# Optimization experiments

Measured on AMD Instinct MI355X. Metric: run time of the kernel, lower is better.

Reference implementation:

```python
import jax, jax.numpy as jnp
import numpy as np

# Forest of B perfect binary trees, depth D levels, M = 2**D - 1 nodes/tree.
B, D, H, X, VOCAB, NCLS = 32, 12, 256, 256, 32000, 20
M = 2 ** D - 1          # 4095 nodes per tree
N = B * M               # 131040 total nodes


def setup_inputs() -> dict:
    key = jax.random.key(0)
    ks = jax.random.split(key, 9)
    x = jax.random.randint(ks[0], (N,), 0, VOCAB, dtype=jnp.int32)
    # leaves are the last level of each tree: in-tree index >= 2**(D-1)-1
    leaf = (jnp.arange(M) >= 2 ** (D - 1) - 1).astype(jnp.int32)
    x_mask = jnp.tile(leaf, B)  # [N] int32, 1 on leaves, 0 on internal nodes
    s = 0.02
    Emb = jax.random.normal(ks[1], (VOCAB, X), jnp.float32) * s
    W_iou = jax.random.normal(ks[2], (3 * H, X), jnp.float32) * s
    b_iou = jnp.zeros((3 * H,), jnp.float32)
    U_iou = jax.random.normal(ks[3], (3 * H, H), jnp.float32) * s
    U_f = jax.random.normal(ks[4], (H, H), jnp.float32) * s
    b_f = jnp.ones((H,), jnp.float32)  # forget-gate bias init
    W_out = jax.random.normal(ks[5], (NCLS, H), jnp.float32) * s
    b_out = jnp.zeros((NCLS,), jnp.float32)
    return {"x": x, "x_mask": x_mask, "Emb": Emb, "W_iou": W_iou,
            "b_iou": b_iou, "U_iou": U_iou, "U_f": U_f, "b_f": b_f,
            "W_out": W_out, "b_out": b_out}


def reference(x, x_mask, Emb, W_iou, b_iou, U_iou, U_f, b_f, W_out, b_out):
    # input_module: embedding applied to masked ids, result masked again
    x_emb = Emb[x * x_mask] * x_mask[:, None].astype(Emb.dtype)      # [N, X]
    xiou = (x_emb @ W_iou.T).reshape(B, M, 3 * H)                    # W_iou * x per node
    h_sum = jnp.zeros((B, M, H), Emb.dtype)    # sum of children h (childsum)
    fc_sum = jnp.zeros((B, M, H), Emb.dtype)   # sum_k f_k * c_k from children
    h_all = jnp.zeros((B, M, H), Emb.dtype)
    # topological propagation: leaves (deepest level) -> roots
    for l in range(D - 1, -1, -1):
        s_, e_ = 2 ** l - 1, 2 ** (l + 1) - 1  # static in-tree level slice
        iou = xiou[:, s_:e_] + h_sum[:, s_:e_] @ U_iou.T + b_iou
        i, o, u = jnp.split(iou, 3, axis=-1)
        c = jax.nn.sigmoid(i) * jnp.tanh(u) + fc_sum[:, s_:e_]
        h = jax.nn.sigmoid(o) * jnp.tanh(c)
        h_all = h_all.at[:, s_:e_].set(h)
        if l > 0:
            f = jax.nn.sigmoid(h @ U_f.T + b_f)          # per-child forget gate
            parents = (np.arange(s_, e_) - 1) // 2       # static parent indices
            h_sum = h_sum.at[:, parents].add(h)
            fc_sum = fc_sum.at[:, parents].add(f * c)
    # output_module applied to all node states
    return h_all.reshape(N, H) @ W_out.T + b_out                    # [N, NCLS]
```

## Files before the change

### kernel.cpp

```cpp
#include <hip/hip_runtime.h>

#define B_TREES 32
#define DEPTH   12
#define M_NODES 4095
#define N_NODES (B_TREES * M_NODES)
#define HDIM    256
#define VOCAB   32000
#define NCLS    20
#define LEAFROWS 65536
#define LDSH_S 20

typedef _Float16 f16;
typedef _Float16 f16x8 __attribute__((ext_vector_type(8)));
typedef _Float16 f16x4 __attribute__((ext_vector_type(4)));
typedef _Float16 f16x2 __attribute__((ext_vector_type(2)));
typedef float    f32x4 __attribute__((ext_vector_type(4)));

__device__ __forceinline__ float sigf(float x)      { return 1.0f / (1.0f + __expf(-x)); }
__device__ __forceinline__ float tanh_fast(float x) { return 1.0f - 2.0f / (1.0f + __expf(2.0f * x)); }

__global__ __launch_bounds__(256) void cvt_kernel(
    const float4* __restrict__ Emb,  const float4* __restrict__ Wiou,
    const float4* __restrict__ Uiou, const float4* __restrict__ Uf,
    const float4* __restrict__ Wout,
    f16x4* __restrict__ Emb16,  f16x4* __restrict__ Wiou16,
    f16x4* __restrict__ Uiou16, f16x4* __restrict__ Uf16,
    f16x4* __restrict__ Wout16)
{
    int i = blockIdx.x * 256 + threadIdx.x;
    if (i < VOCAB * HDIM / 4) {
        float4 v = Emb[i];
        f16x4 r; r[0] = (f16)v.x; r[1] = (f16)v.y; r[2] = (f16)v.z; r[3] = (f16)v.w;
        Emb16[i] = r;
    }
    if (i < 768 * HDIM / 4) {
        float4 v = Wiou[i];
        f16x4 r; r[0] = (f16)v.x; r[1] = (f16)v.y; r[2] = (f16)v.z; r[3] = (f16)v.w;
        Wiou16[i] = r;
        float4 u = Uiou[i];
        f16x4 s; s[0] = (f16)u.x; s[1] = (f16)u.y; s[2] = (f16)u.z; s[3] = (f16)u.w;
        Uiou16[i] = s;
    }
    if (i < HDIM * HDIM / 4) {
        float4 v = Uf[i];
        f16x4 r; r[0] = (f16)v.x; r[1] = (f16)v.y; r[2] = (f16)v.z; r[3] = (f16)v.w;
        Uf16[i] = r;
    }
    if (i < 32 * HDIM / 4) {
        int row = i >> 6;
        f16x4 r = {};
        if (row < NCLS) {
            float4 v = Wout[i];
            r[0] = (f16)v.x; r[1] = (f16)v.y; r[2] = (f16)v.z; r[3] = (f16)v.w;
        }
        Wout16[i] = r;
    }
}

#define LEAF_TPW 8
__global__ __launch_bounds__(256) void leaf_kernel(
    const int* __restrict__ x, const f16* __restrict__ Emb16,
    const f16* __restrict__ Wiou16, const float* __restrict__ b_iou,
    f16* __restrict__ h16, f16* __restrict__ cT)
{
    __shared__ f16 wlds[1536 * 8];
    __shared__ f16 ldsh[4][16 * LDSH_S];

    const int tid  = threadIdx.x;
    const int lane = tid & 63;
    const int w    = tid >> 6;
    const int quad = lane >> 4;
    const int l15  = lane & 15;
    const int qk   = quad * 8;
    const int cb0  = blockIdx.y * 16;

    #pragma unroll
    for (int i = 0; i < 6; ++i) {
        int f = i * 256 + tid;
        int mat = f >> 9, r = f & 511, ks = r >> 6, q = (r >> 4) & 3, c = r & 15;
        *(f16x8*)(wlds + f * 8) = *(const f16x8*)(Wiou16 +
            (mat * 256 + cb0 + c) * HDIM + ks * 32 + q * 8);
    }
    __syncthreads();

    const float bi = b_iou[cb0 + l15];
    const float bo = b_iou[256 + cb0 + l15];
    const float bu = b_iou[512 + cb0 + l15];

    const int row0 = (blockIdx.x * 4 + w) * (LEAF_TPW * 16);

    int nodeRow = (row0 >> 11) * M_NODES + 2047 + (row0 & 2047);
    int embBase = x[nodeRow + l15] * HDIM;
    f16x8 a[8];
    #pragma unroll
    for (int ks = 0; ks < 8; ++ks)
        a[ks] = *(const f16x8*)(Emb16 + embBase + ks * 32 + qk);

    for (int rt = 0; rt < LEAF_TPW; ++rt) {
        const int rw = row0 + rt * 16;
        const int curNode = nodeRow;
        f16x8 ac[8];
        #pragma unroll
        for (int ks = 0; ks < 8; ++ks) ac[ks] = a[ks];

        if (rt + 1 < LEAF_TPW) {
            const int rwn = rw + 16;
            nodeRow = (rwn >> 11) * M_NODES + 2047 + (rwn & 2047);
            embBase = x[nodeRow + l15] * HDIM;
            #pragma unroll
            for (int ks = 0; ks < 8; ++ks)
                a[ks] = *(const f16x8*)(Emb16 + embBase + ks * 32 + qk);
        }

        f32x4 acc[3] = {};
        #pragma unroll
        for (int ks = 0; ks < 8; ++ks) {
            #pragma unroll
            for (int mat = 0; mat < 3; ++mat) {
                f16x8 wf = *(const f16x8*)(wlds +
                    ((mat * 8 + ks) * 64 + quad * 16 + l15) * 8);
                acc[mat] = __builtin_amdgcn_mfma_f32_16x16x32_f16(
                    ac[ks], wf, acc[mat], 0, 0, 0);
            }
        }

        f16x4 cv;
        #pragma unroll
        for (int r = 0; r < 4; ++r) {
            float i_ = acc[0][r] + bi;
            float o_ = acc[1][r] + bo;
            float u_ = acc[2][r] + bu;
            float c  = sigf(i_) * tanh_fast(u_);
            float h  = sigf(o_) * tanh_fast(c);
            cv[r] = (f16)c;
            ldsh[w][(quad * 4 + r) * LDSH_S + l15] = (f16)h;
        }
        *(f16x4*)(cT + (cb0 + l15) * LEAFROWS + rw + quad * 4) = cv;

        {
            int row_l = lane >> 2, cpos = (lane & 3) * 4;
            f16x4 v = *(const f16x4*)(&ldsh[w][row_l * LDSH_S + cpos]);
            *(f16x4*)(h16 + (curNode + row_l) * HDIM + cb0 + cpos) = v;
        }
    }
}

__global__ __launch_bounds__(256) void fused_level_kernel(
    const f16* __restrict__ Uiou16, const f16* __restrict__ Uf16,
    const float* __restrict__ b_iou, const float* __restrict__ b_f,
    f16* __restrict__ h16, const f16* __restrict__ cT_child,
    f16* __restrict__ cT_parent, int l, int rows_p, int tpw)
{
    __shared__ f16 wlds[2048 * 8];
    __shared__ f16 ldsh[4][16 * LDSH_S];

    const int tid  = threadIdx.x;
    const int lane = tid & 63;
    const int w    = tid >> 6;
    const int quad = lane >> 4;
    const int l15  = lane & 15;
    const int qk   = quad * 8;
    const int cb0  = blockIdx.y * 16;

    #pragma unroll
    for (int i = 0; i < 8; ++i) {
        int f = i * 256 + tid;
        int mat = f >> 9, r = f & 511, ks = r >> 6, q = (r >> 4) & 3, c = r & 15;
        const f16* src = (mat == 0)
            ? (Uf16 + (cb0 + c) * HDIM + ks * 32 + q * 8)
            : (Uiou16 + ((mat - 1) * 256 + cb0 + c) * HDIM + ks * 32 + q * 8);
        *(f16x8*)(wlds + f * 8) = *(const f16x8*)src;
    }
    __syncthreads();

    const float bi  = b_iou[cb0 + l15];
    const float bo  = b_iou[256 + cb0 + l15];
    const float bu  = b_iou[512 + cb0 + l15];
    const float bfv = b_f[cb0 + l15];
    const int lc = l + 1;
    const int maskc = (1 << lc) - 1;
    const int maskp = (1 << l) - 1;
    const int rows_c = rows_p * 2;

    const int p0 = blockIdx.x * (tpw * 64);

    for (int pt = 0; pt < tpw; ++pt) {
        const int pw = p0 + (pt * 4 + w) * 16;
        if (pw >= rows_p) continue;
        const int cw = 2 * pw;

        int childBase0, childBase1;
        {
            int cl0 = cw + l15;
            childBase0 = ((cl0 >> lc) * M_NODES + maskc + (cl0 & maskc)) * HDIM;
            int cl1 = cw + 16 + l15;
            childBase1 = ((cl1 >> lc) * M_NODES + maskc + (cl1 & maskc)) * HDIM;
        }

        f32x4 accf0 = {}, accf1 = {};
        f32x4 au0[3] = {}, au1[3] = {};
        #pragma unroll
        for (int ks = 0; ks < 8; ++ks) {
            const int k0 = ks * 32 + qk;
            f16x8 a0 = *(const f16x8*)(h16 + childBase0 + k0);
            f16x8 a1 = *(const f16x8*)(h16 + childBase1 + k0);
            f16x8 wfF = *(const f16x8*)(wlds + (ks * 64 + quad * 16 + l15) * 8);
            accf0 = __builtin_amdgcn_mfma_f32_16x16x32_f16(a0, wfF, accf0, 0, 0, 0);
            accf1 = __builtin_amdgcn_mfma_f32_16x16x32_f16(a1, wfF, accf1, 0, 0, 0);
            #pragma unroll
            for (int m = 0; m < 3; ++m) {
                f16x8 wm = *(const f16x8*)(wlds +
                    (((m + 1) * 8 + ks) * 64 + quad * 16 + l15) * 8);
                au0[m] = __builtin_amdgcn_mfma_f32_16x16x32_f16(a0, wm, au0[m], 0, 0, 0);
                au1[m] = __builtin_amdgcn_mfma_f32_16x16x32_f16(a1, wm, au1[m], 0, 0, 0);
            }
        }

        #pragma unroll
        for (int s = 0; s < 2; ++s) {
            const f32x4& af = s ? accf1 : accf0;
            const f32x4* au = s ? au1 : au0;
            const int csr = cw + s * 16;
            f16x4 cc = *(const f16x4*)(cT_child +
                (cb0 + l15) * rows_c + csr + quad * 4);
            f16x2 cpack;
            #pragma unroll
            for (int pr = 0; pr < 2; ++pr) {
                float f0 = sigf(af[2 * pr]     + bfv);
                float f1 = sigf(af[2 * pr + 1] + bfv);
                float fc = f0 * (float)cc[2 * pr] + f1 * (float)cc[2 * pr + 1];
                float i_ = au[0][2 * pr] + au[0][2 * pr + 1] + bi;
                float o_ = au[1][2 * pr] + au[1][2 * pr + 1] + bo;
                float u_ = au[2][2 * pr] + au[2][2 * pr + 1] + bu;
                float c  = sigf(i_) * tanh_fast(u_) + fc;
                float h  = sigf(o_) * tanh_fast(c);
                cpack[pr] = (f16)c;
                ldsh[w][(s * 8 + quad * 2 + pr) * LDSH_S + l15] = (f16)h;
            }
            *(f16x2*)(cT_parent + (cb0 + l15) * rows_p + pw + s * 8 + quad * 2) = cpack;
        }

        {
            int prow = lane >> 2, cpos = (lane & 3) * 4;
            int p = pw + prow;
            int b = p >> l, tt = p & maskp;
            int node = b * M_NODES + (1 << l) - 1 + tt;
            f16x4 v = *(const f16x4*)(&ldsh[w][prow * LDSH_S + cpos]);
            *(f16x4*)(h16 + node * HDIM + cb0 + cpos) = v;
        }
    }
}

__global__ __launch_bounds__(256) void out_kernel(
    const f16* __restrict__ h16, const f16* __restrict__ Wout16,
    const float* __restrict__ bout, float* __restrict__ out)
{
    const int lane = threadIdx.x & 63;
    const int w    = threadIdx.x >> 6;
    const int quad = lane >> 4;
    const int l15  = lane & 15;
    const int qk   = quad * 8;

    f16x8 wfk[2][8];
    #pragma unroll
    for (int cf = 0; cf < 2; ++cf)
        #pragma unroll
        for (int ks = 0; ks < 8; ++ks)
            wfk[cf][ks] = *(const f16x8*)(Wout16 +
                (cf * 16 + l15) * HDIM + ks * 32 + qk);
    float bo[2];
    #pragma unroll
    for (int cf = 0; cf < 2; ++cf) {
        int col = cf * 16 + l15;
        bo[cf] = bout[col < NCLS ? col : 0];
    }

    const int tile0  = blockIdx.x * 16;
    const int ntotal = N_NODES / 16;
    const int tend   = (tile0 + 16 < ntotal) ? 16 : (ntotal - tile0);

    for (int rt = w; rt < tend; rt += 4) {
        const int rw = (tile0 + rt) * 16;
        f32x4 acc[2] = {};
        #pragma unroll
        for (int ks = 0; ks < 8; ++ks) {
            f16x8 a = *(const f16x8*)(h16 + (rw + l15) * HDIM + ks * 32 + qk);
            #pragma unroll
            for (int cf = 0; cf < 2; ++cf)
                acc[cf] = __builtin_amdgcn_mfma_f32_16x16x32_f16(
                    a, wfk[cf][ks], acc[cf], 0, 0, 0);
        }
        #pragma unroll
        for (int cf = 0; cf < 2; ++cf) {
            const int col = cf * 16 + l15;
            if (col < NCLS) {
                #pragma unroll
                for (int r = 0; r < 4; ++r)
                    out[(rw + quad * 4 + r) * NCLS + col] = acc[cf][r] + bo[cf];
            }
        }
    }
}

extern "C" void kernel_launch(void* const* d_in, const int* in_sizes, int n_in,
                              void* d_out, int out_size, void* d_ws, size_t ws_size,
                              hipStream_t stream)
{
    const int*   x     = (const int*)d_in[0];
    const float* Emb   = (const float*)d_in[2];
    const float* W_iou = (const float*)d_in[3];
    const float* b_iou = (const float*)d_in[4];
    const float* U_iou = (const float*)d_in[5];
    const float* U_f   = (const float*)d_in[6];
    const float* b_f   = (const float*)d_in[7];
    const float* W_out = (const float*)d_in[8];
    const float* b_out = (const float*)d_in[9];
    float* out = (float*)d_out;

    char* ws = (char*)d_ws;
    size_t off = 0;
    auto take = [&](size_t bytes) -> char* {
        char* p = ws + off; off += (bytes + 255) & ~(size_t)255; return p;
    };
    f16* h16    = (f16*)take((size_t)N_NODES * HDIM * 2);
    f16* cA     = (f16*)take((size_t)HDIM * LEAFROWS * 2);
    f16* cB     = (f16*)take((size_t)HDIM * (LEAFROWS / 2) * 2);
    f16* Emb16  = (f16*)take((size_t)VOCAB * HDIM * 2);
    f16* Wiou16 = (f16*)take((size_t)768 * HDIM * 2);
    f16* Uiou16 = (f16*)take((size_t)768 * HDIM * 2);
    f16* Uf16   = (f16*)take((size_t)HDIM * HDIM * 2);
    f16* Wout16 = (f16*)take((size_t)32 * HDIM * 2);

    cvt_kernel<<<VOCAB * HDIM / 4 / 256, 256, 0, stream>>>(
        (const float4*)Emb, (const float4*)W_iou, (const float4*)U_iou,
        (const float4*)U_f, (const float4*)W_out,
        (f16x4*)Emb16, (f16x4*)Wiou16, (f16x4*)Uiou16, (f16x4*)Uf16,
        (f16x4*)Wout16);

    leaf_kernel<<<dim3(LEAFROWS / (4 * 16 * LEAF_TPW), 16), 256, 0, stream>>>(
        x, Emb16, Wiou16, b_iou, h16, cA);

    f16* cin  = cA;
    f16* cout_ = cB;
    for (int l = 10; l >= 0; --l) {
        int rows_p = B_TREES << l;
        int tpw = rows_p / (64 * 128); if (tpw < 1) tpw = 1;
        int gx  = (rows_p + tpw * 64 - 1) / (tpw * 64);
        fused_level_kernel<<<dim3(gx, 16), 256, 0, stream>>>(
            Uiou16, Uf16, b_iou, b_f, h16, cin, cout_, l, rows_p, tpw);
        f16* t = cin; cin = cout_; cout_ = t;
    }

    out_kernel<<<dim3((N_NODES / 16 + 15) / 16), 256, 0, stream>>>(
        h16, Wout16, b_out, out);
}
```

Baseline: 410.3 us.

## Precompute leaf LSTM states per vocabulary token and gather them for leaves

```diff
diff --git a/kernel.cpp b/kernel.cpp
--- a/kernel.cpp
+++ b/kernel.cpp
@@ -57,14 +57,15 @@
     }
 }
 
-#define LEAF_TPW 8
-__global__ __launch_bounds__(256) void leaf_kernel(
-    const int* __restrict__ x, const f16* __restrict__ Emb16,
-    const f16* __restrict__ Wiou16, const float* __restrict__ b_iou,
-    f16* __restrict__ h16, f16* __restrict__ cT)
+#define VTPW 5
+__global__ __launch_bounds__(256) void vocab_kernel(
+    const f16* __restrict__ Emb16, const f16* __restrict__ Wiou16,
+    const float* __restrict__ b_iou,
+    f16* __restrict__ hv, f16* __restrict__ cv)
 {
     __shared__ f16 wlds[1536 * 8];
-    __shared__ f16 ldsh[4][16 * LDSH_S];
+    __shared__ f16 ldshH[4][16 * LDSH_S];
+    __shared__ f16 ldshC[4][16 * LDSH_S];
 
     const int tid  = threadIdx.x;
     const int lane = tid & 63;
@@ -87,29 +88,23 @@
     const float bo = b_iou[256 + cb0 + l15];
     const float bu = b_iou[512 + cb0 + l15];
 
-    const int row0 = (blockIdx.x * 4 + w) * (LEAF_TPW * 16);
-
-    int nodeRow = (row0 >> 11) * M_NODES + 2047 + (row0 & 2047);
-    int embBase = x[nodeRow + l15] * HDIM;
+    const int row0 = (blockIdx.x * 4 + w) * (VTPW * 16);
+
     f16x8 a[8];
     #pragma unroll
     for (int ks = 0; ks < 8; ++ks)
-        a[ks] = *(const f16x8*)(Emb16 + embBase + ks * 32 + qk);
-
-    for (int rt = 0; rt < LEAF_TPW; ++rt) {
+        a[ks] = *(const f16x8*)(Emb16 + (row0 + l15) * HDIM + ks * 32 + qk);
+
+    for (int rt = 0; rt < VTPW; ++rt) {
         const int rw = row0 + rt * 16;
-        const int curNode = nodeRow;
         f16x8 ac[8];
         #pragma unroll
         for (int ks = 0; ks < 8; ++ks) ac[ks] = a[ks];
 
-        if (rt + 1 < LEAF_TPW) {
-            const int rwn = rw + 16;
-            nodeRow = (rwn >> 11) * M_NODES + 2047 + (rwn & 2047);
-            embBase = x[nodeRow + l15] * HDIM;
+        if (rt + 1 < VTPW) {
             #pragma unroll
             for (int ks = 0; ks < 8; ++ks)
-                a[ks] = *(const f16x8*)(Emb16 + embBase + ks * 32 + qk);
+                a[ks] = *(const f16x8*)(Emb16 + (rw + 16 + l15) * HDIM + ks * 32 + qk);
         }
 
         f32x4 acc[3] = {};
@@ -124,7 +119,6 @@
             }
         }
 
-        f16x4 cv;
         #pragma unroll
         for (int r = 0; r < 4; ++r) {
             float i_ = acc[0][r] + bi;
@@ -132,16 +126,117 @@
             float u_ = acc[2][r] + bu;
             float c  = sigf(i_) * tanh_fast(u_);
             float h  = sigf(o_) * tanh_fast(c);
-            cv[r] = (f16)c;
-            ldsh[w][(quad * 4 + r) * LDSH_S + l15] = (f16)h;
-        }
-        *(f16x4*)(cT + (cb0 + l15) * LEAFROWS + rw + quad * 4) = cv;
+            ldshH[w][(quad * 4 + r) * LDSH_S + l15] = (f16)h;
+            ldshC[w][(quad * 4 + r) * LDSH_S + l15] = (f16)c;
+        }
 
         {
             int row_l = lane >> 2, cpos = (lane & 3) * 4;
-            f16x4 v = *(const f16x4*)(&ldsh[w][row_l * LDSH_S + cpos]);
-            *(f16x4*)(h16 + (curNode + row_l) * HDIM + cb0 + cpos) = v;
-        }
+            f16x4 vh = *(const f16x4*)(&ldshH[w][row_l * LDSH_S + cpos]);
+            *(f16x4*)(hv + (rw + row_l) * HDIM + cb0 + cpos) = vh;
+            f16x4 vc = *(const f16x4*)(&ldshC[w][row_l * LDSH_S + cpos]);
+            *(f16x4*)(cv + (rw + row_l) * HDIM + cb0 + cpos) = vc;
+        }
+    }
+}
+
+__global__ __launch_bounds__(256) void vocab_out_kernel(
+    const f16* __restrict__ hv, const f16* __restrict__ Wout16,
+    const float* __restrict__ bout, float* __restrict__ out_v)
+{
+    const int lane = threadIdx.x & 63;
+    const int w    = threadIdx.x >> 6;
+    const int quad = lane >> 4;
+    const int l15  = lane & 15;
+    const int qk   = quad * 8;
+
+    f16x8 wfk[2][8];
+    #pragma unroll
+    for (int cf = 0; cf < 2; ++cf)
+        #pragma unroll
+        for (int ks = 0; ks < 8; ++ks)
+            wfk[cf][ks] = *(const f16x8*)(Wout16 +
+                (cf * 16 + l15) * HDIM + ks * 32 + qk);
+    float bo[2];
+    #pragma unroll
+    for (int cf = 0; cf < 2; ++cf) {
+        int col = cf * 16 + l15;
+        bo[cf] = bout[col < NCLS ? col : 0];
+    }
+
+    const int tile0 = blockIdx.x * 16;
+
+    for (int rt = w; rt < 16; rt += 4) {
+        const int rw = (tile0 + rt) * 16;
+        f32x4 acc[2] = {};
+        #pragma unroll
+        for (int ks = 0; ks < 8; ++ks) {
+            f16x8 a = *(const f16x8*)(hv + (rw + l15) * HDIM + ks * 32 + qk);
+            #pragma unroll
+            for (int cf = 0; cf < 2; ++cf)
+                acc[cf] = __builtin_amdgcn_mfma_f32_16x16x32_f16(
+                    a, wfk[cf][ks], acc[cf], 0, 0, 0);
+        }
+        #pragma unroll
+        for (int cf = 0; cf < 2; ++cf) {
+            const int col = cf * 16 + l15;
+            if (col < NCLS) {
+                #pragma unroll
+                for (int r = 0; r < 4; ++r)
+                    out_v[(rw + quad * 4 + r) * NCLS + col] = acc[cf][r] + bo[cf];
+            }
+        }
+    }
+}
+
+__global__ __launch_bounds__(256) void leaf_scatter_kernel(
+    const int* __restrict__ x, const f16* __restrict__ hv,
+    const f16* __restrict__ cv, const float* __restrict__ out_v,
+    f16* __restrict__ h16, f16* __restrict__ cT, float* __restrict__ out)
+{
+    __shared__ int ids[64];
+    __shared__ f16 ldsc[64][HDIM + 8];
+
+    const int tid = threadIdx.x;
+    const int R0  = blockIdx.x * 64;
+
+    if (tid < 64) {
+        int r = R0 + tid;
+        int node = (r >> 11) * M_NODES + 2047 + (r & 2047);
+        ids[tid] = x[node];
+    }
+    __syncthreads();
+
+    const int r    = tid >> 2;
+    const int p    = tid & 3;
+    const int id   = ids[r];
+    const int gr   = R0 + r;
+    const int node = (gr >> 11) * M_NODES + 2047 + (gr & 2047);
+
+    #pragma unroll
+    for (int j = 0; j < 8; ++j) {
+        f16x8 v = *(const f16x8*)(hv + id * HDIM + p * 64 + j * 8);
+        *(f16x8*)(h16 + node * HDIM + p * 64 + j * 8) = v;
+    }
+    #pragma unroll
+    for (int j = 0; j < 8; ++j) {
+        f16x8 v = *(const f16x8*)(cv + id * HDIM + p * 64 + j * 8);
+        *(f16x8*)(&ldsc[r][p * 64 + j * 8]) = v;
+    }
+    #pragma unroll
+    for (int j = 0; j < 5; ++j)
+        out[node * NCLS + p * 5 + j] = out_v[id * NCLS + p * 5 + j];
+
+    __syncthreads();
+
+    {
+        const int c = tid;
+        f16 tmp[64];
+        #pragma unroll
+        for (int rr = 0; rr < 64; ++rr) tmp[rr] = ldsc[rr][c];
+        #pragma unroll
+        for (int j = 0; j < 8; ++j)
+            *(f16x8*)(cT + c * LEAFROWS + R0 + j * 8) = *(const f16x8*)(&tmp[j * 8]);
     }
 }
 
@@ -275,12 +370,11 @@
         bo[cf] = bout[col < NCLS ? col : 0];
     }
 
-    const int tile0  = blockIdx.x * 16;
-    const int ntotal = N_NODES / 16;
-    const int tend   = (tile0 + 16 < ntotal) ? 16 : (ntotal - tile0);
-
-    for (int rt = w; rt < tend; rt += 4) {
-        const int rw = (tile0 + rt) * 16;
+    const int tile0 = blockIdx.x * 16;
+
+    for (int rt = w; rt < 16; rt += 4) {
+        const int tt = tile0 + rt;
+        const int rw = (tt >> 7) * M_NODES + (tt & 127) * 16;
         f32x4 acc[2] = {};
         #pragma unroll
         for (int ks = 0; ks < 8; ++ks) {
@@ -330,6 +424,9 @@
     f16* Uiou16 = (f16*)take((size_t)768 * HDIM * 2);
     f16* Uf16   = (f16*)take((size_t)HDIM * HDIM * 2);
     f16* Wout16 = (f16*)take((size_t)32 * HDIM * 2);
+    f16* cv     = (f16*)take((size_t)VOCAB * HDIM * 2);
+    float* outv = (float*)take((size_t)VOCAB * NCLS * 4);
+    f16* hv     = cB;
 
     cvt_kernel<<<VOCAB * HDIM / 4 / 256, 256, 0, stream>>>(
         (const float4*)Emb, (const float4*)W_iou, (const float4*)U_iou,
@@ -337,8 +434,14 @@
         (f16x4*)Emb16, (f16x4*)Wiou16, (f16x4*)Uiou16, (f16x4*)Uf16,
         (f16x4*)Wout16);
 
-    leaf_kernel<<<dim3(LEAFROWS / (4 * 16 * LEAF_TPW), 16), 256, 0, stream>>>(
-        x, Emb16, Wiou16, b_iou, h16, cA);
+    vocab_kernel<<<dim3(VOCAB / (4 * 16 * VTPW), 16), 256, 0, stream>>>(
+        Emb16, Wiou16, b_iou, hv, cv);
+
+    vocab_out_kernel<<<dim3(VOCAB / 16 / 16), 256, 0, stream>>>(
+        hv, Wout16, b_out, outv);
+
+    leaf_scatter_kernel<<<dim3(LEAFROWS / 64), 256, 0, stream>>>(
+        x, hv, cv, outv, h16, cA, out);
 
     f16* cin  = cA;
     f16* cout_ = cB;
@@ -351,6 +454,6 @@
         f16* t = cin; cin = cout_; cout_ = t;
     }
 
-    out_kernel<<<dim3((N_NODES / 16 + 15) / 16), 256, 0, stream>>>(
+    out_kernel<<<dim3(32 * 128 / 16), 256, 0, stream>>>(
         h16, Wout16, b_out, out);
 }
```

New measurement: 410.1 us. About the same (-0.1%).
